# Performance work log

Hardware: AMD Instinct MI355X
Metric: run time of the kernel (lower is better)

The kernel has to match this reference:

```python
import jax, jax.numpy as jnp
import numpy as np

C = 2048      # in_dim (fixed by Incidence_matrix conv)
P = 8         # patch_size
HW = 64       # feature_size
BN_EPS = 1e-5


def setup_inputs() -> dict:
    key = jax.random.key(0)
    ks = jax.random.split(key, 12)
    B = 4
    x = jax.random.normal(ks[0], (B, C, HW, HW), dtype=jnp.float32)
    s = 0.02
    Wk = jax.random.normal(ks[1], (C // 8, C), dtype=jnp.float32) * s
    bk = jax.random.normal(ks[2], (C // 8,), dtype=jnp.float32) * s
    Wq = jax.random.normal(ks[3], (C // 8, C), dtype=jnp.float32) * s
    bq = jax.random.normal(ks[4], (C // 8,), dtype=jnp.float32) * s
    Wv = jax.random.normal(ks[5], (C, C), dtype=jnp.float32) * s
    bv = jax.random.normal(ks[6], (C,), dtype=jnp.float32) * s
    inc_W = jax.random.normal(ks[7], (256, C), dtype=jnp.float32) * s
    inc_b = jax.random.normal(ks[8], (256,), dtype=jnp.float32) * s
    bn_gamma = jnp.ones((256,), dtype=jnp.float32)
    bn_beta = jnp.zeros((256,), dtype=jnp.float32)
    bn_mean = jax.random.normal(ks[9], (256,), dtype=jnp.float32) * 0.1
    bn_var = jax.random.uniform(ks[10], (256,), dtype=jnp.float32) + 0.5
    return {"x": x, "Wk": Wk, "bk": bk, "Wq": Wq, "bq": bq, "Wv": Wv,
            "bv": bv, "inc_W": inc_W, "inc_b": inc_b, "bn_gamma": bn_gamma,
            "bn_beta": bn_beta, "bn_mean": bn_mean, "bn_var": bn_var}


def _forward(x, Wk, bk, Wq, bq, Wv, bv, inc_W, inc_b, bn_gamma, bn_beta, bn_mean, bn_var):
    B, Cc, H, W = x.shape
    nh, nw = H // P, W // P
    N = nh * nw
    Ck = Cc // 8

    # Incidence branch: 1x1 conv -> BN (eval) -> ReLU
    inc = jnp.einsum('bchw,kc->bkhw', x, inc_W) + inc_b[:, None, None]
    inc = (inc - bn_mean[:, None, None]) * (bn_gamma[:, None, None]
          / jnp.sqrt(bn_var[:, None, None] + BN_EPS)) + bn_beta[:, None, None]
    inc = jax.nn.relu(inc)
    # 4x4 avg/max pool (stride 4), then relu each and add
    inc5 = inc.reshape(B, 256, H // 4, 4, W // 4, 4)
    inc_pool = jax.nn.relu(inc5.mean((3, 5))) + jax.nn.relu(inc5.max((3, 5)))
    inc_flat = inc_pool.reshape(B, 256, -1)[:, :, :N]          # [B,256,N] (only first N cols used)

    # Patchify exactly as torch: rearrange 'b c (h p1)(w p2) -> b (h w)(p1 p2 c)'
    # then each flat (p1 p2 c) vector is reinterpreted (view) as (C,p,p).
    patches = (x.reshape(B, Cc, nh, P, nw, P)
                 .transpose(0, 2, 4, 3, 5, 1)                  # [B,nh,nw,p,p,C]
                 .reshape(B, N, Cc, P, P))                      # faithful scrambled view

    # Shared 1x1 KQV projections over all patches
    K = jnp.einsum('bncpq,kc->bnkpq', patches, Wk) + bk[:, None, None]   # [B,N,C/8,p,p]
    Q = jnp.einsum('bncpq,kc->bnkpq', patches, Wq) + bq[:, None, None]
    V = jnp.einsum('bncpq,kc->bnkpq', patches, Wv) + bv[:, None, None]   # [B,N,C,p,p]

    # Q_block = sum_i Q_i * incidence scalar per channel
    Q_block = jnp.einsum('bnkpq,bkn->bkpq', Q, inc_flat)        # [B,C/8,p,p]

    Jp = Q_block.reshape(B, Ck, P * P).transpose(0, 2, 1)        # [B,p2,C/8]
    Kp = K.reshape(B, N, Ck, P * P)                              # [B,N,C/8,p2]
    scores = jnp.einsum('bxc,bncy->bnxy', Jp, Kp)                # [B,N,p2,p2]
    A = jax.nn.softmax(scores, axis=2)                           # torch softmax dim=1
    Vp = V.reshape(B, N, Cc, P * P)                              # [B,N,C,p2]
    out = jnp.einsum('bncx,bnxy->bncy', Vp, A)                   # [B,N,C,p2]

    # cat along height then view back to [B,C,H,W] (faithful scrambled reshape)
    out = out.transpose(0, 2, 1, 3).reshape(B, Cc, H, W)
    return out + x


def reference(x, Wk, bk, Wq, bq, Wv, bv, inc_W, inc_b, bn_gamma, bn_beta, bn_mean, bn_var):
    return _forward(x, Wk, bk, Wq, bq, Wv, bv, inc_W, inc_b,
                    bn_gamma, bn_beta, bn_mean, bn_var)
```

## Files before the change

### kernel.cpp

```cpp
#include <hip/hip_runtime.h>
#include <cstdint>
#include <cstddef>


typedef _Float16 f16_t;
typedef __attribute__((ext_vector_type(8))) _Float16 f16x8;
typedef __attribute__((ext_vector_type(4))) _Float16 f16x4;
typedef __attribute__((ext_vector_type(4))) float f32x4;

#define GLD16(gsrc, ldst) __builtin_amdgcn_global_load_lds( \
    (__attribute__((address_space(1))) void*)(gsrc),        \
    (__attribute__((address_space(3))) void*)(ldst), 16, 0, 0)

#define SBAR() do { __builtin_amdgcn_sched_barrier(0); \
                    __builtin_amdgcn_s_barrier();      \
                    __builtin_amdgcn_sched_barrier(0); } while (0)

#define LGKM0() do { asm volatile("s_waitcnt lgkmcnt(0)" ::: "memory"); \
                     __builtin_amdgcn_sched_barrier(0); } while (0)

template<int N> __device__ __forceinline__ void wvm() {
  if constexpr (N == 0)      asm volatile("s_waitcnt vmcnt(0)" ::: "memory");
  else if constexpr (N == 2) asm volatile("s_waitcnt vmcnt(2)" ::: "memory");
  else if constexpr (N == 4) asm volatile("s_waitcnt vmcnt(4)" ::: "memory");
  __builtin_amdgcn_sched_barrier(0);
}

__device__ __forceinline__ void split16(float v, f16_t& h, f16_t& l) {
  h = (f16_t)v;
  l = (f16_t)(v - (float)h);
}

__global__ __launch_bounds__(256)
void prep_kernel(const float* __restrict__ Wk, const float* __restrict__ bk,
                 const float* __restrict__ Wq, const float* __restrict__ bq,
                 const float* __restrict__ Wv, const float* __restrict__ incW,
                 f16_t* __restrict__ Wkq_a0, f16_t* __restrict__ Wkq_a1,
                 f16_t* __restrict__ Wv_f,
                 f16_t* __restrict__ incW_a0, f16_t* __restrict__ incW_a1,
                 float* __restrict__ bias_kq)
{
  __shared__ float lds[2048];
  const int row = blockIdx.x;
  const int t = threadIdx.x;
  const float* src;
  f16_t* d0;
  f16_t* d1;
  bool permute = true;
  if (row < 256) {
    src = Wk + (size_t)row * 2048; d0 = Wkq_a0 + (size_t)row * 2048; d1 = Wkq_a1 + (size_t)row * 2048;
  } else if (row < 512) {
    src = Wq + (size_t)(row - 256) * 2048; d0 = Wkq_a0 + (size_t)row * 2048; d1 = Wkq_a1 + (size_t)row * 2048;
  } else if (row < 2560) {
    src = Wv + (size_t)(row - 512) * 2048; d0 = Wv_f + (size_t)(row - 512) * 2048; d1 = nullptr;
  } else {
    src = incW + (size_t)(row - 2560) * 2048; d0 = incW_a0 + (size_t)(row - 2560) * 2048;
    d1 = incW_a1 + (size_t)(row - 2560) * 2048; permute = false;
  }
#pragma unroll
  for (int i = 0; i < 8; ++i) lds[i * 256 + t] = src[i * 256 + t];
  if (row < 512 && t == 0) bias_kq[row] = (row < 256) ? bk[row] : bq[row - 256];
  __syncthreads();
#pragma unroll
  for (int i = 0; i < 8; ++i) {
    int kh = i * 256 + t;
    int cp = permute ? (((kh >> 3) & 7) * 256 + (kh & 7) * 32 + (kh >> 6)) : kh;
    float v = lds[cp];
    f16_t hh, ll;
    split16(v, hh, ll);
    d0[kh] = hh;
    if (d1) d1[kh] = ll;
  }
}

__global__ __launch_bounds__(256)
void gather_kernel(const float* __restrict__ x,
                   f16_t* __restrict__ P0, f16_t* __restrict__ P1)
{
  __shared__ float lds[16][8][68];
  const int bid = blockIdx.x;
  const int b = bid >> 8;
  const int ph = (bid >> 5) & 7;
  const int tqc = (bid >> 2) & 7;
  const int qq = bid & 3;
  const int t = threadIdx.x;
  for (int k = 0; k < 4; ++k) {
    const int chunk = qq * 4 + k;
    const int cbase = tqc * 256 + chunk * 16;
#pragma unroll
    for (int it = 0; it < 8; ++it) {
      int flat = it * 1024 + t * 4;
      int ci = flat >> 9, p1 = (flat >> 6) & 7, w = flat & 63;
      const float4 v = *(const float4*)&x[(((size_t)b * 2048 + cbase + ci) * 64 + ph * 8 + p1) * 64 + w];
      *(float4*)&lds[ci][p1][w] = v;
    }
    __syncthreads();
    const int tq = tqc * 4 + qq;
    const int jb = k * 16;
#pragma unroll
    for (int it2 = 0; it2 < 8; ++it2) {
      int flat2 = it2 * 256 + t;
      int g = flat2 & 15, jp = flat2 >> 4;
      int ji = jp >> 3, pw = jp & 7;
      int p1 = g >> 1, w0 = pw * 8 + (g & 1) * 4;
      const float4 v = *(const float4*)&lds[ji][p1][w0];
      float vv[4] = {v.x, v.y, v.z, v.w};
      f16x4 h, l;
#pragma unroll
      for (int u = 0; u < 4; ++u) {
        f16_t hh, ll;
        split16(vv[u], hh, ll);
        h[u] = hh; l[u] = ll;
      }
      size_t pg = (size_t)(b * 64 + ph * 8 + pw);
      size_t dst = pg * 131072 + (size_t)(jb + ji) * 2048 + tq * 64 + g * 4;
      *(f16x4*)&P0[dst] = h;
      *(f16x4*)&P1[dst] = l;
    }
    __syncthreads();
  }
}

__global__ __launch_bounds__(256)
void xt_kernel(const float* __restrict__ x,
               f16_t* __restrict__ T0, f16_t* __restrict__ T1)
{
  __shared__ float lds[64][65];
  const int bid = blockIdx.x;
  const int b = bid >> 9;
  const int h = (bid >> 5) & 15;
  const int cc = bid & 31;
  const int t = threadIdx.x;
  {
    int ci = t >> 2, w4 = t & 3;
    const float* src = &x[(((size_t)b * 2048 + cc * 64 + ci) * 64 + h) * 64];
#pragma unroll
    for (int it = 0; it < 4; ++it) {
      int w0 = it * 16 + w4 * 4;
      const float4 v = *(const float4*)&src[w0];
      lds[ci][w0 + 0] = v.x; lds[ci][w0 + 1] = v.y;
      lds[ci][w0 + 2] = v.z; lds[ci][w0 + 3] = v.w;
    }
  }
  __syncthreads();
  const int w = t >> 2, cq = t & 3;
  const size_t rowbase = ((size_t)b * 1024 + h * 64 + w) * 2048 + cc * 64 + cq * 16;
  f16x8 H0, H1, L0, L1;
#pragma unroll
  for (int u = 0; u < 8; ++u) {
    f16_t hh, ll;
    split16(lds[cq * 16 + u][w], hh, ll);
    H0[u] = hh; L0[u] = ll;
  }
#pragma unroll
  for (int u = 0; u < 8; ++u) {
    f16_t hh, ll;
    split16(lds[cq * 16 + 8 + u][w], hh, ll);
    H1[u] = hh; L1[u] = ll;
  }
  *(f16x8*)&T0[rowbase] = H0; *(f16x8*)&T0[rowbase + 8] = H1;
  *(f16x8*)&T1[rowbase] = L0; *(f16x8*)&T1[rowbase + 8] = L1;
}

template<int PHASES, int EPI, int SLICES>
__global__ __launch_bounds__(256)
void gemm_kernel(const f16_t* __restrict__ A0, const f16_t* __restrict__ A1,
                 const f16_t* __restrict__ B0, const f16_t* __restrict__ B1,
                 float* __restrict__ Cf, f16_t* __restrict__ Cb,
                 const float* __restrict__ bias, int MB, int ldc)
{
  __shared__ f16_t As[128 * 64];
  __shared__ f16_t Bs[128 * 64];
  const int nwg = gridDim.x;
  const int q = nwg >> 3;
  const int bid = ((int)blockIdx.x & 7) * q + ((int)blockIdx.x >> 3);
  const int tiles = nwg / SLICES;
  const int slice = bid / tiles;
  const int rem = bid % tiles;
  const int nb = rem / MB, mb = rem % MB;
  const int m0 = mb * 128, n0 = nb * 128;
  const int t = threadIdx.x;
  const int lane = t & 63, wv = t >> 6;
  const int wm = (wv >> 1) * 64, wn = (wv & 1) * 64;
  const int l15 = lane & 15, l4 = lane >> 4;

  const f32x4 vzero = {0.f, 0.f, 0.f, 0.f};
  f32x4 acc[4][4];
#pragma unroll
  for (int i = 0; i < 4; ++i)
#pragma unroll
    for (int j = 0; j < 4; ++j) acc[i][j] = vzero;

  constexpr int LOCAL = (32 * PHASES) / SLICES;
  for (int s = 0; s < LOCAL; ++s) {
    const int step = slice * LOCAL + s;
    const int ph = step >> 5;
    const int k0 = (step & 31) << 6;
    const f16_t* Ab = (PHASES == 3 && ph == 2) ? A1 : A0;
    const f16_t* Bb = (PHASES == 3 && ph == 1) ? B1 : B0;
    __syncthreads();
#pragma unroll
    for (int i = 0; i < 4; ++i) {
      int e = i * 2048 + t * 8;
      int row = e >> 6;
      int gl = ((e >> 3) & 7) ^ (row & 7);
      GLD16(Ab + (size_t)(m0 + row) * 2048 + k0 + gl * 8, &As[e]);
    }
#pragma unroll
    for (int i = 0; i < 4; ++i) {
      int e = i * 2048 + t * 8;
      int row = e >> 6;
      int gl = ((e >> 3) & 7) ^ (row & 7);
      GLD16(Bb + (size_t)(n0 + row) * 2048 + k0 + gl * 8, &Bs[e]);
    }
    __syncthreads();
#pragma unroll
    for (int ks = 0; ks < 2; ++ks) {
      f16x8 a[4], bb[4];
#pragma unroll
      for (int i = 0; i < 4; ++i) {
        int r = wm + i * 16 + l15;
        int g = (ks * 4 + l4) ^ (r & 7);
        a[i] = *(const f16x8*)&As[r * 64 + g * 8];
      }
#pragma unroll
      for (int j = 0; j < 4; ++j) {
        int r = wn + j * 16 + l15;
        int g = (ks * 4 + l4) ^ (r & 7);
        bb[j] = *(const f16x8*)&Bs[r * 64 + g * 8];
      }
#pragma unroll
      for (int i = 0; i < 4; ++i)
#pragma unroll
        for (int j = 0; j < 4; ++j)
          acc[i][j] = __builtin_amdgcn_mfma_f32_16x16x32_f16(a[i], bb[j], acc[i][j], 0, 0, 0);
    }
  }

  float* Cp = Cf + (size_t)slice * (size_t)MB * 128 * (size_t)ldc;
#pragma unroll
  for (int i = 0; i < 4; ++i) {
#pragma unroll
    for (int j = 0; j < 4; ++j) {
      int nloc = n0 + wn + j * 16 + l15;
#pragma unroll
      for (int r = 0; r < 4; ++r) {
        int m = m0 + wm + i * 16 + l4 * 4 + r;
        float bsv = (SLICES == 1 || slice == 0) ? bias[m] : 0.f;
        Cp[(size_t)m * ldc + nloc] = acc[i][j][r] + bsv;
      }
    }
  }
}

#define RDA(dst, RH) \
  _Pragma("unroll") for (int i = 0; i < MIQ; ++i) \
  _Pragma("unroll") for (int ks = 0; ks < 2; ++ks) { \
    int r = wm * WTM + (RH) * (WTM / 2) + i * 16 + l15; \
    dst[i][ks] = *(const f16x8*)&lds[cb + r * 64 + (((ks * 4 + l4) ^ (r & 7)) << 3)]; \
  }
#define RDB(dst, CH) \
  _Pragma("unroll") for (int j = 0; j < NJQ; ++j) \
  _Pragma("unroll") for (int ks = 0; ks < 2; ++ks) { \
    int r = wn * WTN + (CH) * (WTN / 2) + j * 16 + l15; \
    dst[j][ks] = *(const f16x8*)&lds[cb + BBASE + r * 64 + (((ks * 4 + l4) ^ (r & 7)) << 3)]; \
  }
#define QMFMA(AR, BR, RH, CH) do { \
  __builtin_amdgcn_s_setprio(1); \
  _Pragma("unroll") for (int ks = 0; ks < 2; ++ks) \
  _Pragma("unroll") for (int i = 0; i < MIQ; ++i) \
  _Pragma("unroll") for (int j = 0; j < NJQ; ++j) \
    acc[(RH) * MIQ + i][(CH) * NJQ + j] = __builtin_amdgcn_mfma_f32_16x16x32_f16( \
        AR[i][ks], BR[j][ks], acc[(RH) * MIQ + i][(CH) * NJQ + j], 0, 0, 0); \
  __builtin_amdgcn_s_setprio(0); } while (0)

template<int NPH, int EPI, int BM, int BN, int WM, int WN, int MBT>
__global__ __launch_bounds__(512, 2)
void gemm8_kernel(const f16_t* __restrict__ A0f, const f16_t* __restrict__ A1f,
                  const f16_t* __restrict__ B0f, const f16_t* __restrict__ B1f,
                  float* __restrict__ Cf, f16_t* __restrict__ Cb,
                  const float* __restrict__ bias, int ldc)
{
  constexpr int WTM = BM / WM, WTN = BN / WN;
  constexpr int MIQ = WTM / 32, NJQ = WTN / 32;
  constexpr int GA = BM / 128, GB = BN / 128;
  constexpr int BBASE = BM * 64;
  constexpr int BUF = (BM + BN) * 64;
  constexpr int NT = 32 * NPH;
  constexpr int VW = 2 * GB;
  __shared__ f16_t lds[2 * BUF];

  const int nwg = gridDim.x;
  const int q = nwg >> 3;
  const int bid = ((int)blockIdx.x & 7) * q + ((int)blockIdx.x >> 3);
  const int mb = bid % MBT, nb = bid / MBT;
  const int m0 = mb * BM, n0 = nb * BN;
  const int tid = threadIdx.x;
  const int lane = tid & 63;
  const int wv = tid >> 6;
  const int wm = wv / WN, wn = wv % WN;
  const int l15 = lane & 15, l4 = lane >> 4;

  auto stageA = [&](int tt, int rg) {
    if (tt >= NT) return;
    const f16_t* s = (NPH == 3 && (tt >> 5) == 2) ? A1f : A0f;
    const int g0 = m0 + rg * (BM / 2);
    const int base = (tt & 1) * BUF + rg * (BM / 2) * 64;
    const int k0 = (tt & 31) << 6;
#pragma unroll
    for (int i = 0; i < GA; ++i) {
      int idx = i * 4096 + tid * 8;
      int r = idx >> 6, sl = (idx >> 3) & 7;
      GLD16(s + (size_t)(g0 + r) * 2048 + k0 + ((sl ^ (r & 7)) << 3), &lds[base + idx]);
    }
  };
  auto stageB = [&](int tt, int rg) {
    if (tt >= NT) return;
    const f16_t* s = (NPH == 3 && (tt >> 5) == 1) ? B1f : B0f;
    const int g0 = n0 + rg * (BN / 2);
    const int base = (tt & 1) * BUF + BBASE + rg * (BN / 2) * 64;
    const int k0 = (tt & 31) << 6;
#pragma unroll
    for (int i = 0; i < GB; ++i) {
      int idx = i * 4096 + tid * 8;
      int r = idx >> 6, sl = (idx >> 3) & 7;
      GLD16(s + (size_t)(g0 + r) * 2048 + k0 + ((sl ^ (r & 7)) << 3), &lds[base + idx]);
    }
  };

  const f32x4 vzero = {0.f, 0.f, 0.f, 0.f};
  f32x4 acc[WTM / 16][WTN / 16];
#pragma unroll
  for (int i = 0; i < WTM / 16; ++i)
#pragma unroll
    for (int j = 0; j < WTN / 16; ++j) acc[i][j] = vzero;

  stageA(0, 0); stageA(0, 1); stageB(0, 0); stageB(0, 1);
  stageB(1, 0); stageB(1, 1);
  wvm<VW>();
  SBAR();

  for (int tt = 0; tt < NT; ++tt) {
    const int cb = (tt & 1) * BUF;
    f16x8 a0[MIQ][2], a1[MIQ][2], b0[NJQ][2], b1[NJQ][2];
    RDA(a0, 0); RDB(b0, 0);
    stageA(tt + 1, 0);
    SBAR(); LGKM0();
    QMFMA(a0, b0, 0, 0);
    SBAR();
    RDB(b1, 1);
    stageA(tt + 1, 1);
    SBAR(); LGKM0();
    QMFMA(a0, b1, 0, 1);
    SBAR();
    RDA(a1, 1);
    stageB(tt + 2, 0);
    SBAR(); LGKM0();
    QMFMA(a1, b0, 1, 0);
    SBAR();
    stageB(tt + 2, 1);
    if (tt < NT - 2) { wvm<VW>(); } else { wvm<0>(); }
    SBAR();
    QMFMA(a1, b1, 1, 1);
    SBAR();
  }

#pragma unroll
  for (int i = 0; i < WTM / 16; ++i) {
#pragma unroll
    for (int j = 0; j < WTN / 16; ++j) {
      int ncol = n0 + wn * WTN + j * 16 + l15;
#pragma unroll
      for (int r = 0; r < 4; ++r) {
        int m = m0 + wm * WTM + i * 16 + l4 * 4 + r;
        float v = acc[i][j][r] + bias[m];
        if (EPI == 0) {
          Cf[(size_t)m * ldc + ncol] = v;
        } else {
          int patch = ncol >> 6, jj = ncol & 63;
          Cb[(size_t)patch * 131072 + (size_t)m * 64 + jj] = (f16_t)v;
        }
      }
    }
  }
}

__global__ void pool_kernel(const float* __restrict__ incout,
                            const float* __restrict__ bnmean, const float* __restrict__ bnvar,
                            const float* __restrict__ gamma, const float* __restrict__ beta,
                            float* __restrict__ incf)
{
  const int blk = blockIdx.x;
  const int b = blk >> 8, k = blk & 255;
  const int n = threadIdx.x;
  const int r = n >> 4, cq = n & 15;
  const float sc = gamma[k] * rsqrtf(bnvar[k] + 1e-5f);
  const float sh = beta[k] - bnmean[k] * sc;
  const size_t PSTR = (size_t)256 * 4096;
  const size_t base = (size_t)k * 4096 + b * 1024 + (r * 4) * 64 + cq * 4;
  float sum = 0.f, mx = 0.f;
#pragma unroll
  for (int dr = 0; dr < 4; ++dr)
#pragma unroll
    for (int dw = 0; dw < 4; ++dw) {
      size_t idx = base + dr * 64 + dw;
      float raw = incout[idx] + incout[idx + PSTR] + incout[idx + 2 * PSTR];
      float v = fmaxf(raw * sc + sh, 0.f);
      sum += v; mx = fmaxf(mx, v);
    }
  incf[(size_t)blk * 64 + n] = sum * (1.f / 16.f) + mx;
}

__global__ void qblock_kernel(const float* __restrict__ KQ,
                              const float* __restrict__ incf,
                              float* __restrict__ Qb)
{
  const int blk = blockIdx.x;
  const int b = blk >> 8, k = blk & 255;
  const int x = threadIdx.x;
  const float* qrow = KQ + (size_t)(256 + k) * 16384 + (size_t)b * 4096;
  const float* ivec = incf + (size_t)blk * 64;
  float a0 = 0.f, a1 = 0.f, a2 = 0.f, a3 = 0.f;
#pragma unroll
  for (int n = 0; n < 16; ++n) {
    a0 += qrow[n * 64 + x] * ivec[n];
    a1 += qrow[(n + 16) * 64 + x] * ivec[n + 16];
    a2 += qrow[(n + 32) * 64 + x] * ivec[n + 32];
    a3 += qrow[(n + 48) * 64 + x] * ivec[n + 48];
  }
  Qb[(size_t)blk * 64 + x] = (a0 + a1) + (a2 + a3);
}

__global__ __launch_bounds__(256)
void scores_kernel(const float* __restrict__ KQ, const float* __restrict__ Qb,
                   f16_t* __restrict__ Asm)
{
  __shared__ float Qs[64 * 64];
  __shared__ float Ks[64 * 64];
  const int pg = blockIdx.x;
  const int b = pg >> 6;
  const int t = threadIdx.x;
  const int y = t >> 2, xg = t & 3;
  float s[16];
#pragma unroll
  for (int i = 0; i < 16; ++i) s[i] = 0.f;
  for (int kc = 0; kc < 4; ++kc) {
    __syncthreads();
#pragma unroll
    for (int i = 0; i < 16; ++i) {
      int idx = i * 256 + t;
      Qs[idx] = Qb[(size_t)b * 16384 + kc * 4096 + idx];
      int kl = idx >> 6, yy = idx & 63;
      Ks[idx] = KQ[(size_t)(kc * 64 + kl) * 16384 + (size_t)pg * 64 + yy];
    }
    __syncthreads();
    float sc[16];
#pragma unroll
    for (int i = 0; i < 16; ++i) sc[i] = 0.f;
    for (int k = 0; k < 64; ++k) {
      float kv = Ks[k * 64 + y];
      const float4* qr = (const float4*)&Qs[k * 64 + xg * 16];
#pragma unroll
      for (int q4 = 0; q4 < 4; ++q4) {
        float4 qv = qr[q4];
        sc[q4 * 4 + 0] += qv.x * kv;
        sc[q4 * 4 + 1] += qv.y * kv;
        sc[q4 * 4 + 2] += qv.z * kv;
        sc[q4 * 4 + 3] += qv.w * kv;
      }
    }
#pragma unroll
    for (int i = 0; i < 16; ++i) s[i] += sc[i];
  }
  float mx = s[0];
#pragma unroll
  for (int i = 1; i < 16; ++i) mx = fmaxf(mx, s[i]);
  mx = fmaxf(mx, __shfl_xor(mx, 1));
  mx = fmaxf(mx, __shfl_xor(mx, 2));
  float p[16], sum = 0.f;
#pragma unroll
  for (int i = 0; i < 16; ++i) { p[i] = expf(s[i] - mx); sum += p[i]; }
  sum += __shfl_xor(sum, 1);
  sum += __shfl_xor(sum, 2);
  const float rinv = 1.f / sum;
#pragma unroll
  for (int i = 0; i < 16; ++i)
    Asm[(size_t)pg * 4096 + y * 64 + xg * 16 + i] = (f16_t)(p[i] * rinv);
}

__global__ __launch_bounds__(256)
void final_kernel(const f16_t* __restrict__ V, const f16_t* __restrict__ Asm,
                  const float* __restrict__ xin, float* __restrict__ out)
{
  __shared__ f16_t Vs[256 * 64];
  __shared__ f16_t Ps[64 * 64];
  const int bid = blockIdx.x;
  const int pg = bid >> 3, cb = bid & 7;
  const int b = pg >> 6, nl = pg & 63;
  const int t = threadIdx.x;
  const int lane = t & 63, wv = t >> 6;
  const int l15 = lane & 15, l4 = lane >> 4;
  const int wm = wv * 64;

#pragma unroll
  for (int i = 0; i < 8; ++i) {
    int e = i * 2048 + t * 8;
    int row = e >> 6;
    int gl = ((e >> 3) & 7) ^ (row & 7);
    GLD16(V + (size_t)pg * 131072 + (size_t)(cb * 256 + row) * 64 + gl * 8, &Vs[e]);
  }
#pragma unroll
  for (int i = 0; i < 2; ++i) {
    int e = i * 2048 + t * 8;
    int row = e >> 6;
    int gl = ((e >> 3) & 7) ^ (row & 7);
    GLD16(Asm + (size_t)pg * 4096 + (size_t)row * 64 + gl * 8, &Ps[e]);
  }
  __syncthreads();

  const f32x4 vzero = {0.f, 0.f, 0.f, 0.f};
  f32x4 acc[4][4];
#pragma unroll
  for (int i = 0; i < 4; ++i)
#pragma unroll
    for (int j = 0; j < 4; ++j) acc[i][j] = vzero;

#pragma unroll
  for (int ks = 0; ks < 2; ++ks) {
    f16x8 a[4], p[4];
#pragma unroll
    for (int i = 0; i < 4; ++i) {
      int r = wm + i * 16 + l15;
      int g = (ks * 4 + l4) ^ (r & 7);
      a[i] = *(const f16x8*)&Vs[r * 64 + g * 8];
    }
#pragma unroll
    for (int j = 0; j < 4; ++j) {
      int r = j * 16 + l15;
      int g = (ks * 4 + l4) ^ (r & 7);
      p[j] = *(const f16x8*)&Ps[r * 64 + g * 8];
    }
#pragma unroll
    for (int i = 0; i < 4; ++i)
#pragma unroll
      for (int j = 0; j < 4; ++j)
        acc[i][j] = __builtin_amdgcn_mfma_f32_16x16x32_f16(a[i], p[j], acc[i][j], 0, 0, 0);
  }

#pragma unroll
  for (int i = 0; i < 4; ++i) {
#pragma unroll
    for (int j = 0; j < 4; ++j) {
      int y = j * 16 + l15;
#pragma unroll
      for (int r = 0; r < 4; ++r) {
        int c = cb * 256 + wm + i * 16 + l4 * 4 + r;
        size_t idx = (((size_t)b * 2048 + c) * 64 + nl) * 64 + y;
        out[idx] = acc[i][j][r] + xin[idx];
      }
    }
  }
}

extern "C" void kernel_launch(void* const* d_in, const int* in_sizes, int n_in,
                              void* d_out, int out_size, void* d_ws, size_t ws_size,
                              hipStream_t stream) {
  const float* x     = (const float*)d_in[0];
  const float* Wk    = (const float*)d_in[1];
  const float* bk    = (const float*)d_in[2];
  const float* Wq    = (const float*)d_in[3];
  const float* bq    = (const float*)d_in[4];
  const float* Wv    = (const float*)d_in[5];
  const float* bv    = (const float*)d_in[6];
  const float* incW  = (const float*)d_in[7];
  const float* incb  = (const float*)d_in[8];
  const float* gamma = (const float*)d_in[9];
  const float* beta  = (const float*)d_in[10];
  const float* bnmean= (const float*)d_in[11];
  const float* bnvar = (const float*)d_in[12];

  char* ws = (char*)d_ws;
  f16_t* Wkq_a0 = (f16_t*)(ws + 0);
  f16_t* Wkq_a1 = (f16_t*)(ws + 2097152);
  f16_t* Wv_f   = (f16_t*)(ws + 4194304);
  f16_t* incW_a0= (f16_t*)(ws + 12582912);
  f16_t* incW_a1= (f16_t*)(ws + 13631488);
  float* biaskq = (float*) (ws + 14680064);
  float* incout = (float*) (ws + 14682112);
  float* incf   = (float*) (ws + 31459328);
  float* Qb     = (float*) (ws + 31721472);
  f16_t* Asm    = (f16_t*)(ws + 31983616);
  float* KQ     = (float*) (ws + 34080768);
  f16_t* xT_a0  = (f16_t*)(ws + 67635200);
  f16_t* xT_a1  = (f16_t*)(ws + 84412416);
  f16_t* P_a0   = (f16_t*)(ws + 101189632);
  f16_t* P_a1   = (f16_t*)(ws + 168298496);
  f16_t* Vbuf   = P_a1;

  prep_kernel<<<2816, 256, 0, stream>>>(Wk, bk, Wq, bq, Wv, incW,
                                        Wkq_a0, Wkq_a1, Wv_f, incW_a0, incW_a1, biaskq);
  gather_kernel<<<1024, 256, 0, stream>>>(x, P_a0, P_a1);
  xt_kernel<<<2048, 256, 0, stream>>>(x, xT_a0, xT_a1);
  gemm_kernel<3, 0, 3><<<192, 256, 0, stream>>>(incW_a0, incW_a1, xT_a0, xT_a1,
                                                incout, nullptr, incb, 2, 4096);
  pool_kernel<<<1024, 64, 0, stream>>>(incout, bnmean, bnvar, gamma, beta, incf);
  gemm8_kernel<3, 0, 256, 128, 4, 2, 2><<<256, 512, 0, stream>>>(
      Wkq_a0, Wkq_a1, P_a0, P_a1, KQ, nullptr, biaskq, 16384);
  qblock_kernel<<<1024, 64, 0, stream>>>(KQ, incf, Qb);
  scores_kernel<<<256, 256, 0, stream>>>(KQ, Qb, Asm);
  gemm8_kernel<1, 1, 256, 256, 2, 4, 8><<<512, 512, 0, stream>>>(
      Wv_f, Wv_f, P_a0, P_a0, nullptr, Vbuf, bv, 64);
  final_kernel<<<2048, 256, 0, stream>>>(Vbuf, Asm, x, (float*)d_out);
}
```

Baseline: 482.7 us.

## Add single-buffered V GEMM kernel with higher occupancy and drop epilogue template

The V projection GEMM moves off the double-buffered, software-pipelined gemm8 kernel onto a new gemm1b kernel. The new kernel uses a single 64 KB LDS buffer and launch bounds of 4 blocks per SM, so more workgroups can be resident at once and they can hide each other's latency. Inside each block, loads and MFMAs no longer overlap, since every k-step waits for all of its global loads before computing. gemm8 loses its EPI template parameter and keeps only the fp32 output path.

```diff
diff --git a/kernel.cpp b/kernel.cpp
--- a/kernel.cpp
+++ b/kernel.cpp
@@ -274,12 +274,11 @@
         AR[i][ks], BR[j][ks], acc[(RH) * MIQ + i][(CH) * NJQ + j], 0, 0, 0); \
   __builtin_amdgcn_s_setprio(0); } while (0)
 
-template<int NPH, int EPI, int BM, int BN, int WM, int WN, int MBT>
+template<int NPH, int BM, int BN, int WM, int WN, int MBT>
 __global__ __launch_bounds__(512, 2)
 void gemm8_kernel(const f16_t* __restrict__ A0f, const f16_t* __restrict__ A1f,
                   const f16_t* __restrict__ B0f, const f16_t* __restrict__ B1f,
-                  float* __restrict__ Cf, f16_t* __restrict__ Cb,
-                  const float* __restrict__ bias, int ldc)
+                  float* __restrict__ Cf, const float* __restrict__ bias, int ldc)
 {
   constexpr int WTM = BM / WM, WTN = BN / WN;
   constexpr int MIQ = WTM / 32, NJQ = WTN / 32;
@@ -373,13 +372,79 @@
 #pragma unroll
       for (int r = 0; r < 4; ++r) {
         int m = m0 + wm * WTM + i * 16 + l4 * 4 + r;
+        Cf[(size_t)m * ldc + ncol] = acc[i][j][r] + bias[m];
+      }
+    }
+  }
+}
+
+__global__ __launch_bounds__(512, 4)
+void gemm1b_kernel(const f16_t* __restrict__ Af, const f16_t* __restrict__ Bf,
+                   f16_t* __restrict__ Cb, const float* __restrict__ bias)
+{
+  constexpr int WTM = 128, WTN = 64, MIQ = 4, NJQ = 2;
+  constexpr int BBASE = 16384;
+  __shared__ f16_t lds[32768];
+  const int nwg = gridDim.x;
+  const int q = nwg >> 3;
+  const int bid = ((int)blockIdx.x & 7) * q + ((int)blockIdx.x >> 3);
+  const int mb = bid & 7, nb = bid >> 3;
+  const int m0 = mb * 256, n0 = nb * 256;
+  const int tid = threadIdx.x;
+  const int lane = tid & 63;
+  const int wv = tid >> 6;
+  const int wm = wv >> 2, wn = wv & 3;
+  const int l15 = lane & 15, l4 = lane >> 4;
+  const int cb = 0;
+
+  const f32x4 vzero = {0.f, 0.f, 0.f, 0.f};
+  f32x4 acc[8][4];
+#pragma unroll
+  for (int i = 0; i < 8; ++i)
+#pragma unroll
+    for (int j = 0; j < 4; ++j) acc[i][j] = vzero;
+
+  for (int tt = 0; tt < 32; ++tt) {
+    const int k0 = tt << 6;
+#pragma unroll
+    for (int i = 0; i < 4; ++i) {
+      int idx = i * 4096 + tid * 8;
+      int r = idx >> 6, sl = (idx >> 3) & 7;
+      GLD16(Af + (size_t)(m0 + r) * 2048 + k0 + ((sl ^ (r & 7)) << 3), &lds[idx]);
+    }
+#pragma unroll
+    for (int i = 0; i < 4; ++i) {
+      int idx = i * 4096 + tid * 8;
+      int r = idx >> 6, sl = (idx >> 3) & 7;
+      GLD16(Bf + (size_t)(n0 + r) * 2048 + k0 + ((sl ^ (r & 7)) << 3), &lds[BBASE + idx]);
+    }
+    wvm<0>();
+    SBAR();
+    f16x8 a0[MIQ][2], a1[MIQ][2], b0[NJQ][2], b1[NJQ][2];
+    RDA(a0, 0); RDB(b0, 0);
+    LGKM0();
+    QMFMA(a0, b0, 0, 0);
+    RDB(b1, 1);
+    LGKM0();
+    QMFMA(a0, b1, 0, 1);
+    RDA(a1, 1);
+    LGKM0();
+    QMFMA(a1, b0, 1, 0);
+    QMFMA(a1, b1, 1, 1);
+    SBAR();
+  }
+
+#pragma unroll
+  for (int i = 0; i < 8; ++i) {
+#pragma unroll
+    for (int j = 0; j < 4; ++j) {
+      int ncol = n0 + wn * WTN + j * 16 + l15;
+#pragma unroll
+      for (int r = 0; r < 4; ++r) {
+        int m = m0 + wm * WTM + i * 16 + l4 * 4 + r;
         float v = acc[i][j][r] + bias[m];
-        if (EPI == 0) {
-          Cf[(size_t)m * ldc + ncol] = v;
-        } else {
-          int patch = ncol >> 6, jj = ncol & 63;
-          Cb[(size_t)patch * 131072 + (size_t)m * 64 + jj] = (f16_t)v;
-        }
+        int patch = ncol >> 6, jj = ncol & 63;
+        Cb[(size_t)patch * 131072 + (size_t)m * 64 + jj] = (f16_t)v;
       }
     }
   }
@@ -604,11 +669,10 @@
   gemm_kernel<3, 0, 3><<<192, 256, 0, stream>>>(incW_a0, incW_a1, xT_a0, xT_a1,
                                                 incout, nullptr, incb, 2, 4096);
   pool_kernel<<<1024, 64, 0, stream>>>(incout, bnmean, bnvar, gamma, beta, incf);
-  gemm8_kernel<3, 0, 256, 128, 4, 2, 2><<<256, 512, 0, stream>>>(
-      Wkq_a0, Wkq_a1, P_a0, P_a1, KQ, nullptr, biaskq, 16384);
+  gemm8_kernel<3, 256, 128, 4, 2, 2><<<256, 512, 0, stream>>>(
+      Wkq_a0, Wkq_a1, P_a0, P_a1, KQ, biaskq, 16384);
   qblock_kernel<<<1024, 64, 0, stream>>>(KQ, incf, Qb);
   scores_kernel<<<256, 256, 0, stream>>>(KQ, Qb, Asm);
-  gemm8_kernel<1, 1, 256, 256, 2, 4, 8><<<512, 512, 0, stream>>>(
-      Wv_f, Wv_f, P_a0, P_a0, nullptr, Vbuf, bv, 64);
+  gemm1b_kernel<<<512, 512, 0, stream>>>(Wv_f, P_a0, Vbuf, bv);
   final_kernel<<<2048, 256, 0, stream>>>(Vbuf, Asm, x, (float*)d_out);
 }
```

Result: slower. 1.534 ms (+217.9%).
